# Kernel optimization log

Hardware: AMD Instinct MI355X
Metric: run time of the kernel (lower is better)

The kernel has to match this reference:

```python
import jax, jax.numpy as jnp
import numpy as np

PATCH_SIZE = 128
NUM_PATCHES = 4


def setup_inputs() -> dict:
    key = jax.random.key(0)
    k1, k2 = jax.random.split(key)
    B, C, H, W = 32, 3, 512, 512
    images = jax.random.normal(k1, (B, C, H, W), dtype=jnp.float32)
    uncertainty_maps = jax.random.uniform(k2, (B, 1, H, W), dtype=jnp.float32)
    return {"images": images, "uncertainty_maps": uncertainty_maps}


def _select_patches(umap):
    """Greedy masked-argmax patch selection on one [H, W] uncertainty map.
    Returns coords [NUM_PATCHES, 4] int32 as (x1, y1, x2, y2)."""
    H, W = umap.shape
    eps = min(PATCH_SIZE, H // 2, W // 2)   # effective patch size (static)
    half = eps // 2
    margin = max(eps // 4, 1)
    ys = jnp.arange(H)[:, None]
    xs = jnp.arange(W)[None, :]

    def fix(a1, a2, L):
        # enforce window of exactly `eps` when clipped at the border
        small = (a2 - a1) < eps
        a2n = jnp.where(a1 == 0, jnp.minimum(L, a1 + eps), a2)
        a1n = jnp.where(a1 == 0, a1, jnp.maximum(0, a2 - eps))
        return jnp.where(small, a1n, a1), jnp.where(small, a2n, a2)

    def step(mask, _):
        masked = jnp.where(mask, -jnp.inf, umap)
        idx = jnp.argmax(masked)            # row-major first-max, same as np.ma.argmax
        yc = idx // W
        xc = idx % W
        x1 = jnp.maximum(0, xc - half)
        x2 = jnp.minimum(W, xc + half)
        y1 = jnp.maximum(0, yc - half)
        y2 = jnp.minimum(H, yc + half)
        x1, x2 = fix(x1, x2, W)
        y1, y2 = fix(y1, y2, H)
        # suppress selected region plus margin (clamping implicit in comparisons)
        box = (ys >= y1 - margin) & (ys < y2 + margin) & (xs >= x1 - margin) & (xs < x2 + margin)
        coords = jnp.stack([x1, y1, x2, y2]).astype(jnp.int32)
        return mask | box, coords

    _, coords = jax.lax.scan(step, jnp.zeros((H, W), dtype=bool), None, length=NUM_PATCHES)
    return coords  # [NUM_PATCHES, 4]


def _extract(images, coords):
    B, C, H, W = images.shape
    eps = min(PATCH_SIZE, H // 2, W // 2)

    def crop_one(img, c):
        # img [C,H,W], c = (x1,y1,x2,y2); window is always exactly eps x eps
        p = jax.lax.dynamic_slice(img, (0, c[1], c[0]), (C, eps, eps))
        if eps != PATCH_SIZE:
            # bilinear, matches F.interpolate(align_corners=False)
            p = jax.image.resize(p, (C, PATCH_SIZE, PATCH_SIZE), method="bilinear")
        return p

    return jax.vmap(jax.vmap(crop_one, in_axes=(None, 0)), in_axes=(0, 0))(images, coords)


def reference(images, uncertainty_maps):
    coords = jax.vmap(_select_patches)(uncertainty_maps[:, 0])   # [B, N, 4] int32
    patches = _extract(images, coords)                           # [B, N, C, P, P]
    return patches, coords.astype(jnp.float32)
```

## Files before the change

kernel.cpp:

```cpp
#include <hip/hip_runtime.h>
#include <math.h>
#include <float.h>

#define BN 32
#define CH 3
#define HH 512
#define WW 512
#define NP 4
#define EPS 128
#define HALF 64
#define MARGIN 32

#define NT 4096
#define PATCH_ELEMS (BN * NP * CH * EPS * EPS)
#define F4_PER_MAP (NP * CH * EPS * EPS / 4)
#define NSLICE 16
#define F4_PER_SLICE (F4_PER_MAP / NSLICE)
#define K1_NTHR 256
#define K1_NBLK (BN * NT / K1_NTHR)

typedef float nf4 __attribute__((ext_vector_type(4)));


__global__ __launch_bounds__(K1_NTHR)
void tile_scan(const float* __restrict__ umaps, float2* __restrict__ tiles,
               float2* __restrict__ l2g)
{
    const int g  = blockIdx.x * K1_NTHR + threadIdx.x;
    const int b  = g >> 12;
    const int t  = g & (NT - 1);
    const int tx = t & 63, ty = t >> 6;
    const float* __restrict__ um = umaps + (size_t)b * HH * WW;
    const int x0 = tx << 3, y0 = ty << 3;
    float bv = -INFINITY; int bi = 0x7fffffff;
    #pragma unroll
    for (int r = 0; r < 8; ++r) {
        const int rowbase = (y0 + r) * WW + x0;
        const float4 a = *(const float4*)(um + rowbase);
        const float4 c = *(const float4*)(um + rowbase + 4);
        if (a.x > bv) { bv = a.x; bi = rowbase + 0; }
        if (a.y > bv) { bv = a.y; bi = rowbase + 1; }
        if (a.z > bv) { bv = a.z; bi = rowbase + 2; }
        if (a.w > bv) { bv = a.w; bi = rowbase + 3; }
        if (c.x > bv) { bv = c.x; bi = rowbase + 4; }
        if (c.y > bv) { bv = c.y; bi = rowbase + 5; }
        if (c.z > bv) { bv = c.z; bi = rowbase + 6; }
        if (c.w > bv) { bv = c.w; bi = rowbase + 7; }
    }
    tiles[g] = make_float2(bv, __int_as_float(bi));
    float rv = bv; int ri = bi;
    #pragma unroll
    for (int off = 32; off > 0; off >>= 1) {
        const float ov = __shfl_down(rv, off);
        const int   oi = __shfl_down(ri, off);
        if (ov > rv || (ov == rv && oi < ri)) { rv = ov; ri = oi; }
    }
    const int lane = threadIdx.x & 63;
    if (lane == 0) l2g[b * 64 + ty] = make_float2(rv, __int_as_float(ri));
}

__global__ __launch_bounds__(1024)
void select_extract(const float* __restrict__ images,
                    const float* __restrict__ umaps,
                    const float2* __restrict__ tiles,
                    const float2* __restrict__ l2g,
                    float* __restrict__ out)
{
    const int tid   = threadIdx.x;
    const int lane  = tid & 63;
    const int wave  = tid >> 6;
    const int b     = blockIdx.x & (BN - 1);
    const int slice = blockIdx.x >> 5;
    const int nwant = slice >> 2;
    const float* __restrict__ um = umaps + (size_t)b * HH * WW;
    float* coords_out = out + PATCH_ELEMS;

    __shared__ float2   tvi[NT];
    __shared__ float2   l2[64];
    __shared__ unsigned dirty[128];
    __shared__ int      boxes[NP][4];
    __shared__ int      spx1, spy1;

    if (nwant == 0) {
        if (wave == 0) {
            const float2 e = l2g[b * 64 + lane];
            float v = e.x; int ix = __float_as_int(e.y);
            #pragma unroll
            for (int off = 32; off > 0; off >>= 1) {
                const float ov = __shfl_down(v, off);
                const int   oi = __shfl_down(ix, off);
                if (ov > v || (ov == v && oi < ix)) { v = ov; ix = oi; }
            }
            ix = __shfl(ix, 0);
            if (lane == 0) {
                const int yc = ix >> 9, xc = ix & 511;
                int x1 = max(0, xc - HALF), x2 = min(WW, xc + HALF);
                int y1 = max(0, yc - HALF), y2 = min(HH, yc + HALF);
                if (x2 - x1 < EPS) { if (x1 == 0) x2 = EPS; else x1 = x2 - EPS; }
                if (y2 - y1 < EPS) { if (y1 == 0) y2 = EPS; else y1 = y2 - EPS; }
                spx1 = x1; spy1 = y1;
            }
        }
        __syncthreads();
    } else {
        {
            const float4* __restrict__ src = (const float4*)(tiles + (size_t)b * NT);
            float4* dst = (float4*)tvi;
            dst[tid]        = src[tid];
            dst[tid + 1024] = src[tid + 1024];
        }
        if (tid < 64)  l2[tid] = l2g[b * 64 + tid];
        if (tid < 128) dirty[tid] = 0u;
        if (tid < NP)  { boxes[tid][0] = 0; boxes[tid][1] = 0; boxes[tid][2] = 0; boxes[tid][3] = 0; }
        __syncthreads();

        for (int k = 0; k <= nwant; ++k) {
            if (wave == 0) {
                for (;;) {
                    const float2 e = l2[lane];
                    float v = e.x; int ix = __float_as_int(e.y);
                    #pragma unroll
                    for (int off = 32; off > 0; off >>= 1) {
                        const float ov = __shfl_down(v, off);
                        const int   oi = __shfl_down(ix, off);
                        if (ov > v || (ov == v && oi < ix)) { v = ov; ix = oi; }
                    }
                    ix = __shfl(ix, 0);
                    const int t = ((ix >> 12) << 6) | ((ix & 511) >> 3);
                    const bool isdirty = (dirty[t >> 5] >> (t & 31)) & 1u;
                    if (!isdirty) {
                        if (lane == 0) {
                            const int yc = ix >> 9, xc = ix & 511;
                            int x1 = max(0, xc - HALF), x2 = min(WW, xc + HALF);
                            int y1 = max(0, yc - HALF), y2 = min(HH, yc + HALF);
                            if (x2 - x1 < EPS) { if (x1 == 0) x2 = EPS; else x1 = x2 - EPS; }
                            if (y2 - y1 < EPS) { if (y1 == 0) y2 = EPS; else y1 = y2 - EPS; }
                            boxes[k][0] = max(x1 - MARGIN, 0);
                            boxes[k][1] = min(x2 + MARGIN, WW);
                            boxes[k][2] = max(y1 - MARGIN, 0);
                            boxes[k][3] = min(y2 + MARGIN, HH);
                            if (k == nwant) { spx1 = x1; spy1 = y1; }
                            if (slice == NSLICE - 1) {
                                const int o = (b * NP + k) * 4;
                                coords_out[o + 0] = (float)x1;
                                coords_out[o + 1] = (float)y1;
                                coords_out[o + 2] = (float)x2;
                                coords_out[o + 3] = (float)y2;
                            }
                        }
                        break;
                    }
                    const int ty = t >> 6, tx = t & 63;
                    const int y = (ty << 3) + (lane >> 3), x = (tx << 3) + (lane & 7);
                    float pv = um[y * WW + x];
                    int   pi = y * WW + x;
                    bool m = false;
                    #pragma unroll
                    for (int j = 0; j < NP; ++j)
                        m |= (y >= boxes[j][2] && y < boxes[j][3] &&
                              x >= boxes[j][0] && x < boxes[j][1]);
                    if (m) { pv = -INFINITY; pi = 0x7fffffff; }
                    float nv = pv; int ni = pi;
                    #pragma unroll
                    for (int off = 32; off > 0; off >>= 1) {
                        const float ov = __shfl_down(nv, off);
                        const int   oi = __shfl_down(ni, off);
                        if (ov > nv || (ov == nv && oi < ni)) { nv = ov; ni = oi; }
                    }
                    nv = __shfl(nv, 0); ni = __shfl(ni, 0);
                    if (lane == 0) {
                        tvi[t] = make_float2(nv, __int_as_float(ni));
                        dirty[t >> 5] &= ~(1u << (t & 31));
                    }
                    const float2 e2 = tvi[(ty << 6) + lane];
                    float rv2; int ri2;
                    if (lane == tx) { rv2 = nv; ri2 = ni; }
                    else            { rv2 = e2.x; ri2 = __float_as_int(e2.y); }
                    #pragma unroll
                    for (int off = 32; off > 0; off >>= 1) {
                        const float ov = __shfl_down(rv2, off);
                        const int   oi = __shfl_down(ri2, off);
                        if (ov > rv2 || (ov == rv2 && oi < ri2)) { rv2 = ov; ri2 = oi; }
                    }
                    if (lane == 0) l2[ty] = make_float2(rv2, __int_as_float(ri2));
                }
            }
            __syncthreads();

            if (k == nwant) break;

            const int ex1 = boxes[k][0], ex2 = boxes[k][1];
            const int ey1 = boxes[k][2], ey2 = boxes[k][3];
            const int tx1 = ex1 >> 3, tx2 = (ex2 - 1) >> 3;
            const int ty1 = ey1 >> 3, ty2 = (ey2 - 1) >> 3;
            const int wt  = tx2 - tx1 + 1;
            const int nt2 = wt * (ty2 - ty1 + 1);
            if (tid < nt2) {
                const int tx = tx1 + tid % wt;
                const int ty = ty1 + tid / wt;
                const int t  = (ty << 6) + tx;
                const int X1 = tx << 3, Y1 = ty << 3;
                if (X1 >= ex1 && X1 + 8 <= ex2 && Y1 >= ey1 && Y1 + 8 <= ey2)
                    tvi[t] = make_float2(-INFINITY, __int_as_float(0x7fffffff));
                else
                    atomicOr(&dirty[t >> 5], 1u << (t & 31));
            }
            __syncthreads();

            for (int r = ty1 + wave; r <= ty2; r += 16) {
                const float2 e = tvi[(r << 6) + lane];
                float v = e.x; int ix = __float_as_int(e.y);
                #pragma unroll
                for (int off = 32; off > 0; off >>= 1) {
                    const float ov = __shfl_down(v, off);
                    const int   oi = __shfl_down(ix, off);
                    if (ov > v || (ov == v && oi < ix)) { v = ov; ix = oi; }
                }
                if (lane == 0) l2[r] = make_float2(v, __int_as_float(ix));
            }
            __syncthreads();
        }
    }

    const int x1 = spx1, y1 = spy1;
    nf4* __restrict__ out4 = (nf4*)out;
    #pragma unroll
    for (int it = 0; it < 3; ++it) {
        const int il  = slice * F4_PER_SLICE + (it << 10) + tid;
        const int nc  = il >> 12;
        const int c   = nc - nwant * 3;
        const int py  = (il >> 5) & 127;
        const int px0 = (il & 31) << 2;

        const float* __restrict__ src =
            images + (((size_t)b * CH + c) * HH + (y1 + py)) * WW + x1 + px0;
        const nf4 v = { src[0], src[1], src[2], src[3] };
        __builtin_nontemporal_store(v, &out4[(size_t)b * F4_PER_MAP + il]);
    }
}

extern "C" void kernel_launch(void* const* d_in, const int* in_sizes, int n_in,
                              void* d_out, int out_size, void* d_ws, size_t ws_size,
                              hipStream_t stream) {
    const float* images = (const float*)d_in[0];
    const float* umaps  = (const float*)d_in[1];
    float* out          = (float*)d_out;
    float2* tiles       = (float2*)d_ws;
    float2* l2g         = tiles + (size_t)BN * NT;

    tile_scan<<<K1_NBLK, K1_NTHR, 0, stream>>>(umaps, tiles, l2g);
    select_extract<<<BN * NSLICE, 1024, 0, stream>>>(images, umaps, tiles, l2g, out);
}
```

Baseline: 168.8 us.

## Lazily load tile maxima per row and fuse box suppression into row rescan

Blocks that run the greedy selection no longer copy all 4096 tile entries from global memory into LDS up front. A row is fetched from global only when it is first touched by a suppression box, and a rowvalid flag marks rows already resident in LDS. The separate per-tile masking pass, its atomics and one barrier are folded into the row rescan, which sets dirty bits with a wave ballot. The image gather also switches from four scalar loads to a single 4-float load declared with 4-byte alignment. The cost is extra per-row branching and possible uncached global reads inside the serial selection loop.

```diff
diff --git a/kernel.cpp b/kernel.cpp
--- a/kernel.cpp
+++ b/kernel.cpp
@@ -19,7 +19,7 @@
 #define K1_NTHR 256
 #define K1_NBLK (BN * NT / K1_NTHR)
 
-typedef float nf4 __attribute__((ext_vector_type(4)));
+typedef float f4v __attribute__((ext_vector_type(4), aligned(4)));
 
 
 __global__ __launch_bounds__(K1_NTHR)
@@ -73,11 +73,13 @@
     const int slice = blockIdx.x >> 5;
     const int nwant = slice >> 2;
     const float* __restrict__ um = umaps + (size_t)b * HH * WW;
+    const float2* __restrict__ tg = tiles + (size_t)b * NT;
     float* coords_out = out + PATCH_ELEMS;
 
     __shared__ float2   tvi[NT];
     __shared__ float2   l2[64];
     __shared__ unsigned dirty[128];
+    __shared__ int      rowvalid[64];
     __shared__ int      boxes[NP][4];
     __shared__ int      spx1, spy1;
 
@@ -103,13 +105,7 @@
         }
         __syncthreads();
     } else {
-        {
-            const float4* __restrict__ src = (const float4*)(tiles + (size_t)b * NT);
-            float4* dst = (float4*)tvi;
-            dst[tid]        = src[tid];
-            dst[tid + 1024] = src[tid + 1024];
-        }
-        if (tid < 64)  l2[tid] = l2g[b * 64 + tid];
+        if (tid < 64)  { l2[tid] = l2g[b * 64 + tid]; rowvalid[tid] = 0; }
         if (tid < 128) dirty[tid] = 0u;
         if (tid < NP)  { boxes[tid][0] = 0; boxes[tid][1] = 0; boxes[tid][2] = 0; boxes[tid][3] = 0; }
         __syncthreads();
@@ -126,8 +122,8 @@
                         if (ov > v || (ov == v && oi < ix)) { v = ov; ix = oi; }
                     }
                     ix = __shfl(ix, 0);
-                    const int t = ((ix >> 12) << 6) | ((ix & 511) >> 3);
-                    const bool isdirty = (dirty[t >> 5] >> (t & 31)) & 1u;
+                    const int tt = ((ix >> 12) << 6) | ((ix & 511) >> 3);
+                    const bool isdirty = (dirty[tt >> 5] >> (tt & 31)) & 1u;
                     if (!isdirty) {
                         if (lane == 0) {
                             const int yc = ix >> 9, xc = ix & 511;
@@ -150,8 +146,8 @@
                         }
                         break;
                     }
-                    const int ty = t >> 6, tx = t & 63;
-                    const int y = (ty << 3) + (lane >> 3), x = (tx << 3) + (lane & 7);
+                    const int tyd = tt >> 6, txd = tt & 63;
+                    const int y = (tyd << 3) + (lane >> 3), x = (txd << 3) + (lane & 7);
                     float pv = um[y * WW + x];
                     int   pi = y * WW + x;
                     bool m = false;
@@ -169,20 +165,20 @@
                     }
                     nv = __shfl(nv, 0); ni = __shfl(ni, 0);
                     if (lane == 0) {
-                        tvi[t] = make_float2(nv, __int_as_float(ni));
-                        dirty[t >> 5] &= ~(1u << (t & 31));
-                    }
-                    const float2 e2 = tvi[(ty << 6) + lane];
+                        tvi[tt] = make_float2(nv, __int_as_float(ni));
+                        dirty[tt >> 5] &= ~(1u << (tt & 31));
+                    }
+                    const float2 e2 = tvi[(tyd << 6) + lane];
                     float rv2; int ri2;
-                    if (lane == tx) { rv2 = nv; ri2 = ni; }
-                    else            { rv2 = e2.x; ri2 = __float_as_int(e2.y); }
+                    if (lane == txd) { rv2 = nv; ri2 = ni; }
+                    else             { rv2 = e2.x; ri2 = __float_as_int(e2.y); }
                     #pragma unroll
                     for (int off = 32; off > 0; off >>= 1) {
                         const float ov = __shfl_down(rv2, off);
                         const int   oi = __shfl_down(ri2, off);
                         if (ov > rv2 || (ov == rv2 && oi < ri2)) { rv2 = ov; ri2 = oi; }
                     }
-                    if (lane == 0) l2[ty] = make_float2(rv2, __int_as_float(ri2));
+                    if (lane == 0) l2[tyd] = make_float2(rv2, __int_as_float(ri2));
                 }
             }
             __syncthreads();
@@ -191,39 +187,41 @@
 
             const int ex1 = boxes[k][0], ex2 = boxes[k][1];
             const int ey1 = boxes[k][2], ey2 = boxes[k][3];
-            const int tx1 = ex1 >> 3, tx2 = (ex2 - 1) >> 3;
             const int ty1 = ey1 >> 3, ty2 = (ey2 - 1) >> 3;
-            const int wt  = tx2 - tx1 + 1;
-            const int nt2 = wt * (ty2 - ty1 + 1);
-            if (tid < nt2) {
-                const int tx = tx1 + tid % wt;
-                const int ty = ty1 + tid / wt;
-                const int t  = (ty << 6) + tx;
-                const int X1 = tx << 3, Y1 = ty << 3;
-                if (X1 >= ex1 && X1 + 8 <= ex2 && Y1 >= ey1 && Y1 + 8 <= ey2)
-                    tvi[t] = make_float2(-INFINITY, __int_as_float(0x7fffffff));
-                else
-                    atomicOr(&dirty[t >> 5], 1u << (t & 31));
-            }
-            __syncthreads();
-
             for (int r = ty1 + wave; r <= ty2; r += 16) {
-                const float2 e = tvi[(r << 6) + lane];
+                const int base = r << 6;
+                float2 e;
+                if (rowvalid[r]) e = tvi[base + lane];
+                else             e = tg[base + lane];
                 float v = e.x; int ix = __float_as_int(e.y);
+                const int X1 = lane << 3, Y1 = r << 3;
+                const bool cov = (X1 >= ex1 && X1 + 8 <= ex2 &&
+                                  Y1 >= ey1 && Y1 + 8 <= ey2);
+                const bool ovl = (X1 < ex2 && X1 + 8 > ex1 &&
+                                  Y1 < ey2 && Y1 + 8 > ey1);
+                if (cov) { v = -INFINITY; ix = 0x7fffffff; }
+                const unsigned long long dm = __ballot(ovl && !cov);
+                tvi[base + lane] = make_float2(v, __int_as_float(ix));
+                if (lane == 0) {
+                    dirty[2 * r]     |= (unsigned)dm;
+                    dirty[2 * r + 1] |= (unsigned)(dm >> 32);
+                    rowvalid[r] = 1;
+                }
+                float rv = v; int ri = ix;
                 #pragma unroll
                 for (int off = 32; off > 0; off >>= 1) {
-                    const float ov = __shfl_down(v, off);
-                    const int   oi = __shfl_down(ix, off);
-                    if (ov > v || (ov == v && oi < ix)) { v = ov; ix = oi; }
+                    const float ov = __shfl_down(rv, off);
+                    const int   oi = __shfl_down(ri, off);
+                    if (ov > rv || (ov == rv && oi < ri)) { rv = ov; ri = oi; }
                 }
-                if (lane == 0) l2[r] = make_float2(v, __int_as_float(ix));
+                if (lane == 0) l2[r] = make_float2(rv, __int_as_float(ri));
             }
             __syncthreads();
         }
     }
 
     const int x1 = spx1, y1 = spy1;
-    nf4* __restrict__ out4 = (nf4*)out;
+    f4v* __restrict__ out4 = (f4v*)out;
     #pragma unroll
     for (int it = 0; it < 3; ++it) {
         const int il  = slice * F4_PER_SLICE + (it << 10) + tid;
@@ -234,7 +232,7 @@
 
         const float* __restrict__ src =
             images + (((size_t)b * CH + c) * HH + (y1 + py)) * WW + x1 + px0;
-        const nf4 v = { src[0], src[1], src[2], src[3] };
+        const f4v v = *(const f4v*)src;
         __builtin_nontemporal_store(v, &out4[(size_t)b * F4_PER_MAP + il]);
     }
 }
```

Measured after the change: 170.5 us. Within noise of the previous version (+1.0%).
